# Kernel tuning notes

Hardware: AMD Instinct MI355X
Metric: run time of the kernel (lower is better)

The kernel has to match this reference:

```python
import jax, jax.numpy as jnp
import numpy as np

B, N, K, D = 2, 4096, 20, 128
PH = 8          # pos_mlp hidden dim
AH = 4 * D      # attn_mlp hidden dim (attn_mlp_hidden_mult=4)


def setup_inputs() -> dict:
    key = jax.random.key(0)
    ks = jax.random.split(key, 12)
    s = 0.02
    f32 = jnp.float32
    return {
        "x": jax.random.normal(ks[0], (B, N, 3), f32),
        "pos": jax.random.normal(ks[1], (B, N, 3), f32),
        # linear1/2/3 (torch Linear: y = x @ W.T + b)
        "W1": jax.random.normal(ks[2], (D, 3), f32) * s,  "b1": jnp.zeros((D,), f32),
        "W2": jax.random.normal(ks[3], (D, D), f32) * s,  "b2": jnp.zeros((D,), f32),
        "W3": jax.random.normal(ks[4], (D, D), f32) * s,  "b3": jnp.zeros((D,), f32),
        # PointTransformerLayer params
        "Wqkv": jax.random.normal(ks[5], (3 * D, D), f32) * s,          # to_qkv, no bias
        "Wp1": jax.random.normal(ks[6], (PH, 3), f32) * s,  "bp1": jnp.zeros((PH,), f32),
        "Wp2": jax.random.normal(ks[7], (D, PH), f32) * s,  "bp2": jnp.zeros((D,), f32),
        "Wa1": jax.random.normal(ks[8], (AH, D), f32) * s,  "ba1": jnp.zeros((AH,), f32),
        "Wa2": jax.random.normal(ks[9], (D, AH), f32) * s,  "ba2": jnp.zeros((D,), f32),
    }


def reference(x, pos, W1, b1, W2, b2, W3, b3, Wqkv,
              Wp1, bp1, Wp2, bp2, Wa1, ba1, Wa2, ba2):
    h = x @ W1.T + b1            # [B,N,D] linear1
    h1 = h @ W2.T + b2           # [B,N,D] linear2

    # --- PointTransformerLayer (lucidrains, KNN vector attention) ---
    qkv = h1 @ Wqkv.T            # [B,N,3D]
    q, k, v = jnp.split(qkv, 3, axis=-1)

    # squared pairwise distances and K nearest neighbors (self included)
    d2 = jnp.sum((pos[:, :, None, :] - pos[:, None, :, :]) ** 2, axis=-1)  # [B,N,N]
    _, idx = jax.lax.top_k(-d2, K)                                          # [B,N,K]

    gather = jax.vmap(lambda arr, ind: arr[ind])  # per-batch gather -> [B,N,K,*]
    kn = gather(k, idx)          # [B,N,K,D]
    vn = gather(v, idx)          # [B,N,K,D]
    pn = gather(pos, idx)        # [B,N,K,3]

    rel = pos[:, :, None, :] - pn                                   # [B,N,K,3]
    pe = jax.nn.relu(rel @ Wp1.T + bp1) @ Wp2.T + bp2               # pos_mlp [B,N,K,D]

    vn = vn + pe
    sim = jax.nn.relu((q[:, :, None, :] - kn + pe) @ Wa1.T + ba1) @ Wa2.T + ba2  # attn_mlp
    attn = jax.nn.softmax(sim, axis=2)                              # softmax over neighbors
    agg = jnp.sum(attn * vn, axis=2)                                # [B,N,D]

    return h + (agg @ W3.T + b3)  # residual: x + linear3(x1)
```

## Files before the change

kernel.cpp:

```cpp
#include <hip/hip_runtime.h>
#include <stdint.h>

#define BB 2
#define NN 4096
#define KNB 20
#define DD 128
#define PHH 8
#define AHH 512
#define BN (BB*NN)

typedef unsigned short ushort_t;
typedef short bf16x8 __attribute__((ext_vector_type(8)));
typedef float f32x4 __attribute__((ext_vector_type(4)));

__device__ __forceinline__ uint32_t umin32(uint32_t a, uint32_t b) { return a < b ? a : b; }
__device__ __forceinline__ uint32_t umax32(uint32_t a, uint32_t b) { return a > b ? a : b; }

__device__ __forceinline__ ushort_t f2bf(float f) {
    uint32_t x = __float_as_uint(f);
    return (ushort_t)((x + 0x7FFFu + ((x >> 16) & 1u)) >> 16);
}
__device__ __forceinline__ float bf2f(ushort_t u) {
    union { float f; uint32_t i; } c; c.i = ((uint32_t)u) << 16; return c.f;
}
__device__ __forceinline__ uint32_t cvt_pk_bf16(float lo, float hi) {
    uint32_t r;
    asm("v_cvt_pk_bf16_f32 %0, %1, %2" : "=v"(r) : "v"(lo), "v"(hi));
    return r;
}
__device__ __forceinline__ bf16x8 load_bfrag(const float* __restrict__ src) {
    float4 x = *(const float4*)src;
    float4 y = *(const float4*)(src + 4);
    union { bf16x8 v; uint32_t u[4]; } r;
    r.u[0] = cvt_pk_bf16(x.x, x.y);
    r.u[1] = cvt_pk_bf16(x.z, x.w);
    r.u[2] = cvt_pk_bf16(y.x, y.y);
    r.u[3] = cvt_pk_bf16(y.z, y.w);
    return r.v;
}

#define SW256(m, byteInRow) ((m)*256 + ((byteInRow) ^ (((m)&7) << 4)))
#define SW128(m, byteInRow) ((m)*128 + ((byteInRow) ^ (((m)&7) << 4)))

__global__ __launch_bounds__(256) void k_mega(
        const float* __restrict__ x, const float* __restrict__ pos,
        const float* __restrict__ W1, const float* __restrict__ b1,
        const float* __restrict__ W2f, const float* __restrict__ b2,
        const float* __restrict__ Wqkvf,
        const float* __restrict__ Wa1, const float* __restrict__ Wa2,
        float* __restrict__ h, ushort_t* __restrict__ qf,
        ushort_t* __restrict__ kf, ushort_t* __restrict__ vf,
        int* __restrict__ idx, ushort_t* __restrict__ wbf) {
    __shared__ __align__(16) char smem[16896];
    int tid = threadIdx.x, w = tid >> 6, lane = tid & 63;
    int bid = blockIdx.x;

    if (bid < BN/4) {
        int p = bid*4 + w;
        int b = p >> 12;
        float qx = pos[p*3+0], qy = pos[p*3+1], qz = pos[p*3+2];
        const float* pb = pos + (size_t)b*NN*3;
        uint32_t bk[KNB];
        #pragma unroll
        for (int i = 0; i < KNB; ++i) bk[i] = 0xFFFFFFFFu;
        for (int i = 0; i < NN/64; ++i) {
            int j = i*64 + lane;
            float dx = qx - pb[j*3+0];
            float dy = qy - pb[j*3+1];
            float dz = qz - pb[j*3+2];
            float d2 = dx*dx + dy*dy + dz*dz;
            uint32_t key = (__float_as_uint(d2) & 0xFFFFF000u) | (uint32_t)j;
            if (key < bk[KNB-1]) {
                uint32_t c = key;
                #pragma unroll
                for (int t = 0; t < KNB; ++t) {
                    uint32_t lo = umin32(c, bk[t]);
                    uint32_t hi = umax32(c, bk[t]);
                    bk[t] = lo; c = hi;
                }
            }
        }
        for (int r = 0; r < KNB; ++r) {
            uint32_t m = bk[0];
            #pragma unroll
            for (int s = 1; s < 64; s <<= 1)
                m = umin32(m, (uint32_t)__shfl_xor((int)m, s, 64));
            if (lane == 0) idx[(size_t)p*KNB + r] = (int)(m & 0xFFFu);
            bool win = (bk[0] == m);
            #pragma unroll
            for (int t = 0; t < KNB-1; ++t) bk[t] = win ? bk[t+1] : bk[t];
            bk[KNB-1] = win ? 0xFFFFFFFFu : bk[KNB-1];
        }
    } else if (bid < BN/4 + BN/32) {
        float* xs = (float*)(smem + 16384);
        int p0 = (bid - BN/4) * 32;
        if (tid < 96) xs[tid] = x[(size_t)p0*3 + tid];
        __syncthreads();

        #pragma unroll
        for (int it = 0; it < 16; ++it) {
            int lin = it*256 + tid;
            int m = lin >> 7, d = lin & 127;
            float hv = b1[d] + xs[m*3+0]*W1[d*3+0] + xs[m*3+1]*W1[d*3+1] + xs[m*3+2]*W1[d*3+2];
            h[(size_t)(p0+m)*DD + d] = hv;
            *(ushort_t*)&smem[SW256(m, d*2)] = f2bf(hv);
        }
        __syncthreads();

        {
            f32x4 acc[2][2];
            #pragma unroll
            for (int mt = 0; mt < 2; ++mt)
                #pragma unroll
                for (int ntl = 0; ntl < 2; ++ntl) acc[mt][ntl] = (f32x4){0,0,0,0};
            #pragma unroll
            for (int ks = 0; ks < 4; ++ks) {
                int k0 = ks*32 + (lane >> 4)*8;
                bf16x8 aF[2];
                #pragma unroll
                for (int mt = 0; mt < 2; ++mt)
                    aF[mt] = *(const bf16x8*)&smem[SW256(mt*16 + (lane & 15), k0*2)];
                #pragma unroll
                for (int ntl = 0; ntl < 2; ++ntl) {
                    int n = (2*w + ntl)*16 + (lane & 15);
                    bf16x8 bF = load_bfrag(W2f + (size_t)n*DD + k0);
                    #pragma unroll
                    for (int mt = 0; mt < 2; ++mt)
                        acc[mt][ntl] = __builtin_amdgcn_mfma_f32_16x16x32_bf16(aF[mt], bF, acc[mt][ntl], 0, 0, 0);
                }
            }
            #pragma unroll
            for (int ntl = 0; ntl < 2; ++ntl) {
                int n = (2*w + ntl)*16 + (lane & 15);
                float bias = b2[n];
                #pragma unroll
                for (int mt = 0; mt < 2; ++mt)
                    #pragma unroll
                    for (int i = 0; i < 4; ++i) {
                        int m = mt*16 + (lane >> 4)*4 + i;
                        *(ushort_t*)&smem[8192 + SW256(m, n*2)] = f2bf(acc[mt][ntl][i] + bias);
                    }
            }
        }
        __syncthreads();

        {
            f32x4 acc[2][6];
            #pragma unroll
            for (int mt = 0; mt < 2; ++mt)
                #pragma unroll
                for (int ntl = 0; ntl < 6; ++ntl) acc[mt][ntl] = (f32x4){0,0,0,0};
            #pragma unroll
            for (int ks = 0; ks < 4; ++ks) {
                int k0 = ks*32 + (lane >> 4)*8;
                bf16x8 aF[2];
                #pragma unroll
                for (int mt = 0; mt < 2; ++mt)
                    aF[mt] = *(const bf16x8*)&smem[8192 + SW256(mt*16 + (lane & 15), k0*2)];
                #pragma unroll
                for (int ntl = 0; ntl < 6; ++ntl) {
                    int n = (w*6 + ntl)*16 + (lane & 15);
                    bf16x8 bF = load_bfrag(Wqkvf + (size_t)n*DD + k0);
                    #pragma unroll
                    for (int mt = 0; mt < 2; ++mt)
                        acc[mt][ntl] = __builtin_amdgcn_mfma_f32_16x16x32_bf16(aF[mt], bF, acc[mt][ntl], 0, 0, 0);
                }
            }
            #pragma unroll
            for (int ntl = 0; ntl < 6; ++ntl) {
                int n = (w*6 + ntl)*16 + (lane & 15);
                int r = n >> 7, d = n & 127;
                ushort_t* dst = (r == 0) ? qf : (r == 1) ? kf : vf;
                #pragma unroll
                for (int mt = 0; mt < 2; ++mt)
                    #pragma unroll
                    for (int i = 0; i < 4; ++i) {
                        int m = mt*16 + (lane >> 4)*4 + i;
                        dst[(size_t)(p0+m)*DD + d] = f2bf(acc[mt][ntl][i]);
                    }
            }
        }
    } else {
        int base = (bid - (BN/4 + BN/32)) * 2048 + tid * 8;
        const float* src = (base < 65536) ? (Wa1 + base) : (Wa2 + (base - 65536));
        union { ushort_t u[8]; uint4 q; } pk;
        #pragma unroll
        for (int i = 0; i < 8; ++i) pk.u[i] = f2bf(src[i]);
        *(uint4*)&wbf[base] = pk.q;
    }
}

#define XL_OFF 0
#define TL_OFF 20480
#define PH_OFF 30720
#define NIDX_OFF 32000

__global__ __launch_bounds__(256, 4) void k_attn(
        const float* __restrict__ pos,
        const ushort_t* __restrict__ qf, const ushort_t* __restrict__ kf,
        const ushort_t* __restrict__ vf, const int* __restrict__ idx,
        const float* __restrict__ Wp1, const float* __restrict__ bp1,
        const float* __restrict__ Wp2, const float* __restrict__ bp2,
        const ushort_t* __restrict__ Wa1bf, const float* __restrict__ ba1,
        const ushort_t* __restrict__ Wa2bf, const float* __restrict__ ba2,
        float* __restrict__ agg) {
    __shared__ __align__(16) char smem[32320];
    int* nidx = (int*)(smem + NIDX_OFF);

    int tid = threadIdx.x, w = tid >> 6, lane = tid & 63;
    int lg = lane >> 4, c16 = lane & 15;
    int p0 = blockIdx.x * 4, b = p0 >> 12;

    if (tid < 80) nidx[tid] = idx[(size_t)(p0 + tid/20)*KNB + (tid%20)];
    __syncthreads();

    if (tid < 80) {
        int m = tid, g = m / 20;
        int j = nidx[m];
        const float* pq = pos + (size_t)(p0+g)*3;
        const float* pn = pos + (size_t)(b*NN+j)*3;
        float r0 = pq[0]-pn[0], r1 = pq[1]-pn[1], r2 = pq[2]-pn[2];
        union { ushort_t u[8]; uint4 q; } pk;
        #pragma unroll
        for (int jj = 0; jj < PHH; ++jj) {
            float a = bp1[jj] + r0*Wp1[jj*3+0] + r1*Wp1[jj*3+1] + r2*Wp1[jj*3+2];
            pk.u[jj] = f2bf(fmaxf(a, 0.f));
        }
        *(uint4*)&smem[PH_OFF + m*16] = pk.q;
    }
    __syncthreads();

    int dA = w*32 + c16, dB = w*32 + 16 + c16;
    float bp2A = bp2[dA], bp2B = bp2[dB];
    float ba2A = ba2[dA], ba2B = ba2[dB];

    bf16x8 bP0 = {0,0,0,0,0,0,0,0}, bP1 = {0,0,0,0,0,0,0,0};
    if (lg == 0) {
        bP0 = load_bfrag(Wp2 + (size_t)dA*PHH);
        bP1 = load_bfrag(Wp2 + (size_t)dB*PHH);
    }

    float qv[4][2];
    #pragma unroll
    for (int g = 0; g < 4; ++g) {
        qv[g][0] = bf2f(qf[(size_t)(p0+g)*DD + dA]);
        qv[g][1] = bf2f(qf[(size_t)(p0+g)*DD + dB]);
    }

    uint32_t vpe_pk[5][4];

    #pragma unroll
    for (int mt = 0; mt < 5; ++mt) {
        bf16x8 aP = {0,0,0,0,0,0,0,0};
        if (lg == 0) aP = *(const bf16x8*)&smem[PH_OFF + (mt*16 + c16)*16];
        f32x4 accP0 = (f32x4){0,0,0,0}, accP1 = (f32x4){0,0,0,0};
        accP0 = __builtin_amdgcn_mfma_f32_16x16x32_bf16(aP, bP0, accP0, 0, 0, 0);
        accP1 = __builtin_amdgcn_mfma_f32_16x16x32_bf16(aP, bP1, accP1, 0, 0, 0);
        float qsA = (mt==0) ? qv[0][0]
                  : (mt==1) ? (lg>=1 ? qv[1][0] : qv[0][0])
                  : (mt==2) ? (lg>=2 ? qv[2][0] : qv[1][0])
                  : (mt==3) ? (lg==3 ? qv[3][0] : qv[2][0])
                  : qv[3][0];
        float qsB = (mt==0) ? qv[0][1]
                  : (mt==1) ? (lg>=1 ? qv[1][1] : qv[0][1])
                  : (mt==2) ? (lg>=2 ? qv[2][1] : qv[1][1])
                  : (mt==3) ? (lg==3 ? qv[3][1] : qv[2][1])
                  : qv[3][1];
        #pragma unroll
        for (int i = 0; i < 4; ++i) {
            int m = mt*16 + lg*4 + i;
            int j = nidx[m];
            const ushort_t* kr = kf + (size_t)(b*NN+j)*DD;
            const ushort_t* vr = vf + (size_t)(b*NN+j)*DD;
            float peA = accP0[i] + bp2A;
            float peB = accP1[i] + bp2B;
            *(ushort_t*)&smem[XL_OFF + SW256(m, dA*2)] = f2bf(qsA - bf2f(kr[dA]) + peA);
            *(ushort_t*)&smem[XL_OFF + SW256(m, dB*2)] = f2bf(qsB - bf2f(kr[dB]) + peB);
            vpe_pk[mt][i] = cvt_pk_bf16(bf2f(vr[dA]) + peA, bf2f(vr[dB]) + peB);
        }
    }
    __syncthreads();

    f32x4 accS[5][2];
    #pragma unroll
    for (int mt = 0; mt < 5; ++mt)
        #pragma unroll
        for (int ntl = 0; ntl < 2; ++ntl) accS[mt][ntl] = (f32x4){0,0,0,0};

    for (int c = 0; c < 8; ++c) {
        f32x4 accB[5];
        #pragma unroll
        for (int mt = 0; mt < 5; ++mt) accB[mt] = (f32x4){0,0,0,0};
        #pragma unroll
        for (int ks = 0; ks < 4; ++ks) {
            int k0 = ks*32 + lg*8;
            bf16x8 aF[5];
            #pragma unroll
            for (int mt = 0; mt < 5; ++mt)
                aF[mt] = *(const bf16x8*)&smem[XL_OFF + SW256(mt*16 + c16, k0*2)];
            bf16x8 bF = *(const bf16x8*)&Wa1bf[(size_t)(c*64 + w*16 + c16)*DD + k0];
            #pragma unroll
            for (int mt = 0; mt < 5; ++mt)
                accB[mt] = __builtin_amdgcn_mfma_f32_16x16x32_bf16(aF[mt], bF, accB[mt], 0, 0, 0);
        }
        {
            int al = w*16 + c16;
            float bias = ba1[c*64 + al];
            #pragma unroll
            for (int mt = 0; mt < 5; ++mt)
                #pragma unroll
                for (int i = 0; i < 4; ++i) {
                    int m = mt*16 + lg*4 + i;
                    *(ushort_t*)&smem[TL_OFF + SW128(m, al*2)] = f2bf(fmaxf(accB[mt][i] + bias, 0.f));
                }
        }
        __syncthreads();

        #pragma unroll
        for (int ks = 0; ks < 2; ++ks) {
            int k0 = ks*32 + lg*8;
            bf16x8 aF[5];
            #pragma unroll
            for (int mt = 0; mt < 5; ++mt)
                aF[mt] = *(const bf16x8*)&smem[TL_OFF + SW128(mt*16 + c16, k0*2)];
            #pragma unroll
            for (int ntl = 0; ntl < 2; ++ntl) {
                int dd = w*32 + ntl*16 + c16;
                bf16x8 bF = *(const bf16x8*)&Wa2bf[(size_t)dd*AHH + c*64 + k0];
                #pragma unroll
                for (int mt = 0; mt < 5; ++mt)
                    accS[mt][ntl] = __builtin_amdgcn_mfma_f32_16x16x32_bf16(aF[mt], bF, accS[mt][ntl], 0, 0, 0);
            }
        }
        __syncthreads();
    }

    float s_mtA[5], a_mtA[5], s_mtB[5], a_mtB[5];
    #pragma unroll
    for (int mt = 0; mt < 5; ++mt) {
        float sa = 0.f, aa = 0.f, sb = 0.f, ab = 0.f;
        #pragma unroll
        for (int i = 0; i < 4; ++i) {
            float eA = __expf(accS[mt][0][i] + ba2A);
            float eB = __expf(accS[mt][1][i] + ba2B);
            uint32_t pk = vpe_pk[mt][i];
            float vA = bf2f((ushort_t)(pk & 0xFFFFu));
            float vB = bf2f((ushort_t)(pk >> 16));
            sa += eA; aa += eA*vA;
            sb += eB; ab += eB*vB;
        }
        s_mtA[mt] = sa; a_mtA[mt] = aa; s_mtB[mt] = sb; a_mtB[mt] = ab;
    }
    bool eq0 = (lg==0), ge1 = (lg>=1), ge2 = (lg>=2), le1 = (lg<=1), le2 = (lg<=2), eq3 = (lg==3);
    float s0A = s_mtA[0] + (eq0 ? s_mtA[1] : 0.f);
    float s1A = (ge1 ? s_mtA[1] : 0.f) + (le1 ? s_mtA[2] : 0.f);
    float s2A = (ge2 ? s_mtA[2] : 0.f) + (le2 ? s_mtA[3] : 0.f);
    float s3A = (eq3 ? s_mtA[3] : 0.f) + s_mtA[4];
    float a0A = a_mtA[0] + (eq0 ? a_mtA[1] : 0.f);
    float a1A = (ge1 ? a_mtA[1] : 0.f) + (le1 ? a_mtA[2] : 0.f);
    float a2A = (ge2 ? a_mtA[2] : 0.f) + (le2 ? a_mtA[3] : 0.f);
    float a3A = (eq3 ? a_mtA[3] : 0.f) + a_mtA[4];
    float s0B = s_mtB[0] + (eq0 ? s_mtB[1] : 0.f);
    float s1B = (ge1 ? s_mtB[1] : 0.f) + (le1 ? s_mtB[2] : 0.f);
    float s2B = (ge2 ? s_mtB[2] : 0.f) + (le2 ? s_mtB[3] : 0.f);
    float s3B = (eq3 ? s_mtB[3] : 0.f) + s_mtB[4];
    float a0B = a_mtB[0] + (eq0 ? a_mtB[1] : 0.f);
    float a1B = (ge1 ? a_mtB[1] : 0.f) + (le1 ? a_mtB[2] : 0.f);
    float a2B = (ge2 ? a_mtB[2] : 0.f) + (le2 ? a_mtB[3] : 0.f);
    float a3B = (eq3 ? a_mtB[3] : 0.f) + a_mtB[4];

    #define RED2(v) { v += __shfl_xor(v, 16, 64); v += __shfl_xor(v, 32, 64); }
    RED2(s0A) RED2(s1A) RED2(s2A) RED2(s3A)
    RED2(a0A) RED2(a1A) RED2(a2A) RED2(a3A)
    RED2(s0B) RED2(s1B) RED2(s2B) RED2(s3B)
    RED2(a0B) RED2(a1B) RED2(a2B) RED2(a3B)
    #undef RED2

    float myS_A = (lg==0) ? s0A : (lg==1) ? s1A : (lg==2) ? s2A : s3A;
    float myA_A = (lg==0) ? a0A : (lg==1) ? a1A : (lg==2) ? a2A : a3A;
    float myS_B = (lg==0) ? s0B : (lg==1) ? s1B : (lg==2) ? s2B : s3B;
    float myA_B = (lg==0) ? a0B : (lg==1) ? a1B : (lg==2) ? a2B : a3B;
    agg[(size_t)(p0+lg)*DD + dA] = myA_A / myS_A;
    agg[(size_t)(p0+lg)*DD + dB] = myA_B / myS_B;
}

__global__ __launch_bounds__(256) void k_out(
        const float* __restrict__ agg, const float* __restrict__ h,
        const float* __restrict__ W3f, const float* __restrict__ b3,
        float* __restrict__ out) {
    __shared__ __align__(16) char smem[8192];
    int tid = threadIdx.x, w = tid >> 6, lane = tid & 63;
    int p0 = blockIdx.x * 32;

    #pragma unroll
    for (int it = 0; it < 16; ++it) {
        int lin = it*256 + tid;
        int m = lin >> 7, d = lin & 127;
        *(ushort_t*)&smem[SW256(m, d*2)] = f2bf(agg[(size_t)(p0+m)*DD + d]);
    }
    __syncthreads();

    f32x4 acc[2][2];
    #pragma unroll
    for (int mt = 0; mt < 2; ++mt)
        #pragma unroll
        for (int ntl = 0; ntl < 2; ++ntl) acc[mt][ntl] = (f32x4){0,0,0,0};
    #pragma unroll
    for (int ks = 0; ks < 4; ++ks) {
        int k0 = ks*32 + (lane >> 4)*8;
        bf16x8 aF[2];
        #pragma unroll
        for (int mt = 0; mt < 2; ++mt)
            aF[mt] = *(const bf16x8*)&smem[SW256(mt*16 + (lane & 15), k0*2)];
        #pragma unroll
        for (int ntl = 0; ntl < 2; ++ntl) {
            int n = (2*w + ntl)*16 + (lane & 15);
            bf16x8 bF = load_bfrag(W3f + (size_t)n*DD + k0);
            #pragma unroll
            for (int mt = 0; mt < 2; ++mt)
                acc[mt][ntl] = __builtin_amdgcn_mfma_f32_16x16x32_bf16(aF[mt], bF, acc[mt][ntl], 0, 0, 0);
        }
    }
    #pragma unroll
    for (int ntl = 0; ntl < 2; ++ntl) {
        int n = (2*w + ntl)*16 + (lane & 15);
        float bias = b3[n];
        #pragma unroll
        for (int mt = 0; mt < 2; ++mt)
            #pragma unroll
            for (int i = 0; i < 4; ++i) {
                int m = mt*16 + (lane >> 4)*4 + i;
                size_t o = (size_t)(p0+m)*DD + n;
                out[o] = acc[mt][ntl][i] + bias + h[o];
            }
    }
}

extern "C" void kernel_launch(void* const* d_in, const int* in_sizes, int n_in,
                              void* d_out, int out_size, void* d_ws, size_t ws_size,
                              hipStream_t stream) {
    const float* x    = (const float*)d_in[0];
    const float* pos  = (const float*)d_in[1];
    const float* W1   = (const float*)d_in[2];
    const float* b1   = (const float*)d_in[3];
    const float* W2   = (const float*)d_in[4];
    const float* b2   = (const float*)d_in[5];
    const float* W3   = (const float*)d_in[6];
    const float* b3   = (const float*)d_in[7];
    const float* Wqkv = (const float*)d_in[8];
    const float* Wp1  = (const float*)d_in[9];
    const float* bp1  = (const float*)d_in[10];
    const float* Wp2  = (const float*)d_in[11];
    const float* bp2  = (const float*)d_in[12];
    const float* Wa1  = (const float*)d_in[13];
    const float* ba1  = (const float*)d_in[14];
    const float* Wa2  = (const float*)d_in[15];
    const float* ba2  = (const float*)d_in[16];

    float* ws = (float*)d_ws;
    float* h   = ws;
    float* agg = ws + (size_t)BN*DD;
    ushort_t* qf = (ushort_t*)(ws + 2*(size_t)BN*DD);
    ushort_t* kf = qf + (size_t)BN*DD;
    ushort_t* vf = qf + 2*(size_t)BN*DD;
    int* idx = (int*)((char*)d_ws + 14680064);
    ushort_t* wbf = (ushort_t*)((char*)d_ws + 15335424);
    ushort_t* Wa1bf = wbf;
    ushort_t* Wa2bf = wbf + 65536;

    k_mega<<<BN/4 + BN/32 + 64, 256, 0, stream>>>(x, pos, W1, b1, W2, b2, Wqkv,
                                                  Wa1, Wa2, h, qf, kf, vf, idx, wbf);
    k_attn<<<BN/4, 256, 0, stream>>>(pos, qf, kf, vf, idx,
                                     Wp1, bp1, Wp2, bp2, Wa1bf, ba1, Wa2bf, ba2, agg);
    k_out <<<BN/32, 256, 0, stream>>>(agg, h, W3, b3, (float*)d_out);
}
```

Before: 175.1 us.

## Fuse output projection into attention kernel and widen attn-MLP hidden chunk

Removes the separate k_out kernel. Its linear3 projection plus residual now runs at the end of k_attn as a padded 16-row MFMA over the 4 points of each block, using W3 pre-converted to bf16 in k_mega. The attention MLP now processes hidden chunks of 128 instead of 64, which halves the number of barrier rounds at the cost of more LDS (occupancy hint drops from 4 to 3) and more accumulators. s_setprio hints are added around the MFMA sections. The fused output GEMM wastes 12 of 16 MFMA rows but avoids the agg round trip through global memory and one launch.

```diff
diff --git a/kernel.cpp b/kernel.cpp
--- a/kernel.cpp
+++ b/kernel.cpp
@@ -40,7 +40,6 @@
 }
 
 #define SW256(m, byteInRow) ((m)*256 + ((byteInRow) ^ (((m)&7) << 4)))
-#define SW128(m, byteInRow) ((m)*128 + ((byteInRow) ^ (((m)&7) << 4)))
 
 __global__ __launch_bounds__(256) void k_mega(
         const float* __restrict__ x, const float* __restrict__ pos,
@@ -48,6 +47,7 @@
         const float* __restrict__ W2f, const float* __restrict__ b2,
         const float* __restrict__ Wqkvf,
         const float* __restrict__ Wa1, const float* __restrict__ Wa2,
+        const float* __restrict__ W3,
         float* __restrict__ h, ushort_t* __restrict__ qf,
         ushort_t* __restrict__ kf, ushort_t* __restrict__ vf,
         int* __restrict__ idx, ushort_t* __restrict__ wbf) {
@@ -182,7 +182,9 @@
         }
     } else {
         int base = (bid - (BN/4 + BN/32)) * 2048 + tid * 8;
-        const float* src = (base < 65536) ? (Wa1 + base) : (Wa2 + (base - 65536));
+        const float* src = (base < 65536) ? (Wa1 + base)
+                        : (base < 131072) ? (Wa2 + (base - 65536))
+                        : (W3 + (base - 131072));
         union { ushort_t u[8]; uint4 q; } pk;
         #pragma unroll
         for (int i = 0; i < 8; ++i) pk.u[i] = f2bf(src[i]);
@@ -192,10 +194,10 @@
 
 #define XL_OFF 0
 #define TL_OFF 20480
-#define PH_OFF 30720
-#define NIDX_OFF 32000
-
-__global__ __launch_bounds__(256, 4) void k_attn(
+#define PH_OFF 40960
+#define NIDX_OFF 42240
+
+__global__ __launch_bounds__(256, 3) void k_attn(
         const float* __restrict__ pos,
         const ushort_t* __restrict__ qf, const ushort_t* __restrict__ kf,
         const ushort_t* __restrict__ vf, const int* __restrict__ idx,
@@ -203,8 +205,9 @@
         const float* __restrict__ Wp2, const float* __restrict__ bp2,
         const ushort_t* __restrict__ Wa1bf, const float* __restrict__ ba1,
         const ushort_t* __restrict__ Wa2bf, const float* __restrict__ ba2,
-        float* __restrict__ agg) {
-    __shared__ __align__(16) char smem[32320];
+        const ushort_t* __restrict__ W3bf, const float* __restrict__ b3,
+        const float* __restrict__ h, float* __restrict__ out) {
+    __shared__ __align__(16) char smem[42560];
     int* nidx = (int*)(smem + NIDX_OFF);
 
     int tid = threadIdx.x, w = tid >> 6, lane = tid & 63;
@@ -287,10 +290,13 @@
         #pragma unroll
         for (int ntl = 0; ntl < 2; ++ntl) accS[mt][ntl] = (f32x4){0,0,0,0};
 
-    for (int c = 0; c < 8; ++c) {
-        f32x4 accB[5];
-        #pragma unroll
-        for (int mt = 0; mt < 5; ++mt) accB[mt] = (f32x4){0,0,0,0};
+    for (int c = 0; c < 4; ++c) {
+        f32x4 accB[5][2];
+        #pragma unroll
+        for (int mt = 0; mt < 5; ++mt)
+            #pragma unroll
+            for (int ntl = 0; ntl < 2; ++ntl) accB[mt][ntl] = (f32x4){0,0,0,0};
+        __builtin_amdgcn_s_setprio(1);
         #pragma unroll
         for (int ks = 0; ks < 4; ++ks) {
             int k0 = ks*32 + lg*8;
@@ -298,40 +304,47 @@
             #pragma unroll
             for (int mt = 0; mt < 5; ++mt)
                 aF[mt] = *(const bf16x8*)&smem[XL_OFF + SW256(mt*16 + c16, k0*2)];
-            bf16x8 bF = *(const bf16x8*)&Wa1bf[(size_t)(c*64 + w*16 + c16)*DD + k0];
-            #pragma unroll
-            for (int mt = 0; mt < 5; ++mt)
-                accB[mt] = __builtin_amdgcn_mfma_f32_16x16x32_bf16(aF[mt], bF, accB[mt], 0, 0, 0);
-        }
-        {
-            int al = w*16 + c16;
-            float bias = ba1[c*64 + al];
+            #pragma unroll
+            for (int ntl = 0; ntl < 2; ++ntl) {
+                bf16x8 bF = *(const bf16x8*)&Wa1bf[(size_t)(c*128 + w*32 + ntl*16 + c16)*DD + k0];
+                #pragma unroll
+                for (int mt = 0; mt < 5; ++mt)
+                    accB[mt][ntl] = __builtin_amdgcn_mfma_f32_16x16x32_bf16(aF[mt], bF, accB[mt][ntl], 0, 0, 0);
+            }
+        }
+        __builtin_amdgcn_s_setprio(0);
+        #pragma unroll
+        for (int ntl = 0; ntl < 2; ++ntl) {
+            int al = w*32 + ntl*16 + c16;
+            float bias = ba1[c*128 + al];
             #pragma unroll
             for (int mt = 0; mt < 5; ++mt)
                 #pragma unroll
                 for (int i = 0; i < 4; ++i) {
                     int m = mt*16 + lg*4 + i;
-                    *(ushort_t*)&smem[TL_OFF + SW128(m, al*2)] = f2bf(fmaxf(accB[mt][i] + bias, 0.f));
+                    *(ushort_t*)&smem[TL_OFF + SW256(m, al*2)] = f2bf(fmaxf(accB[mt][ntl][i] + bias, 0.f));
                 }
         }
         __syncthreads();
 
-        #pragma unroll
-        for (int ks = 0; ks < 2; ++ks) {
+        __builtin_amdgcn_s_setprio(1);
+        #pragma unroll
+        for (int ks = 0; ks < 4; ++ks) {
             int k0 = ks*32 + lg*8;
             bf16x8 aF[5];
             #pragma unroll
             for (int mt = 0; mt < 5; ++mt)
-                aF[mt] = *(const bf16x8*)&smem[TL_OFF + SW128(mt*16 + c16, k0*2)];
+                aF[mt] = *(const bf16x8*)&smem[TL_OFF + SW256(mt*16 + c16, k0*2)];
             #pragma unroll
             for (int ntl = 0; ntl < 2; ++ntl) {
                 int dd = w*32 + ntl*16 + c16;
-                bf16x8 bF = *(const bf16x8*)&Wa2bf[(size_t)dd*AHH + c*64 + k0];
+                bf16x8 bF = *(const bf16x8*)&Wa2bf[(size_t)dd*AHH + c*128 + k0];
                 #pragma unroll
                 for (int mt = 0; mt < 5; ++mt)
                     accS[mt][ntl] = __builtin_amdgcn_mfma_f32_16x16x32_bf16(aF[mt], bF, accS[mt][ntl], 0, 0, 0);
             }
         }
+        __builtin_amdgcn_s_setprio(0);
         __syncthreads();
     }
 
@@ -380,59 +393,40 @@
     float myA_A = (lg==0) ? a0A : (lg==1) ? a1A : (lg==2) ? a2A : a3A;
     float myS_B = (lg==0) ? s0B : (lg==1) ? s1B : (lg==2) ? s2B : s3B;
     float myA_B = (lg==0) ? a0B : (lg==1) ? a1B : (lg==2) ? a2B : a3B;
-    agg[(size_t)(p0+lg)*DD + dA] = myA_A / myS_A;
-    agg[(size_t)(p0+lg)*DD + dB] = myA_B / myS_B;
-}
-
-__global__ __launch_bounds__(256) void k_out(
-        const float* __restrict__ agg, const float* __restrict__ h,
-        const float* __restrict__ W3f, const float* __restrict__ b3,
-        float* __restrict__ out) {
-    __shared__ __align__(16) char smem[8192];
-    int tid = threadIdx.x, w = tid >> 6, lane = tid & 63;
-    int p0 = blockIdx.x * 32;
-
-    #pragma unroll
-    for (int it = 0; it < 16; ++it) {
-        int lin = it*256 + tid;
-        int m = lin >> 7, d = lin & 127;
-        *(ushort_t*)&smem[SW256(m, d*2)] = f2bf(agg[(size_t)(p0+m)*DD + d]);
-    }
+    float aggA = myA_A / myS_A;
+    float aggB = myA_B / myS_B;
+
+    #pragma unroll
+    for (int z = 0; z < 3; ++z)
+        *(uint32_t*)&smem[XL_OFF + 1024 + (z*256 + tid)*4] = 0u;
+    *(ushort_t*)&smem[XL_OFF + SW256(lg, dA*2)] = f2bf(aggA);
+    *(ushort_t*)&smem[XL_OFF + SW256(lg, dB*2)] = f2bf(aggB);
     __syncthreads();
 
-    f32x4 acc[2][2];
-    #pragma unroll
-    for (int mt = 0; mt < 2; ++mt)
-        #pragma unroll
-        for (int ntl = 0; ntl < 2; ++ntl) acc[mt][ntl] = (f32x4){0,0,0,0};
+    f32x4 accO[2];
+    accO[0] = (f32x4){0,0,0,0}; accO[1] = (f32x4){0,0,0,0};
     #pragma unroll
     for (int ks = 0; ks < 4; ++ks) {
-        int k0 = ks*32 + (lane >> 4)*8;
-        bf16x8 aF[2];
-        #pragma unroll
-        for (int mt = 0; mt < 2; ++mt)
-            aF[mt] = *(const bf16x8*)&smem[SW256(mt*16 + (lane & 15), k0*2)];
+        int k0 = ks*32 + lg*8;
+        bf16x8 aF = *(const bf16x8*)&smem[XL_OFF + SW256(c16, k0*2)];
         #pragma unroll
         for (int ntl = 0; ntl < 2; ++ntl) {
-            int n = (2*w + ntl)*16 + (lane & 15);
-            bf16x8 bF = load_bfrag(W3f + (size_t)n*DD + k0);
-            #pragma unroll
-            for (int mt = 0; mt < 2; ++mt)
-                acc[mt][ntl] = __builtin_amdgcn_mfma_f32_16x16x32_bf16(aF[mt], bF, acc[mt][ntl], 0, 0, 0);
-        }
-    }
-    #pragma unroll
-    for (int ntl = 0; ntl < 2; ++ntl) {
-        int n = (2*w + ntl)*16 + (lane & 15);
-        float bias = b3[n];
-        #pragma unroll
-        for (int mt = 0; mt < 2; ++mt)
+            int n = (w*2 + ntl)*16 + c16;
+            bf16x8 bF = *(const bf16x8*)&W3bf[(size_t)n*DD + k0];
+            accO[ntl] = __builtin_amdgcn_mfma_f32_16x16x32_bf16(aF, bF, accO[ntl], 0, 0, 0);
+        }
+    }
+    if (lg == 0) {
+        #pragma unroll
+        for (int ntl = 0; ntl < 2; ++ntl) {
+            int n = (w*2 + ntl)*16 + c16;
+            float bias = b3[n];
             #pragma unroll
             for (int i = 0; i < 4; ++i) {
-                int m = mt*16 + (lane >> 4)*4 + i;
-                size_t o = (size_t)(p0+m)*DD + n;
-                out[o] = acc[mt][ntl][i] + bias + h[o];
-            }
+                size_t o = (size_t)(p0+i)*DD + n;
+                out[o] = accO[ntl][i] + bias + h[o];
+            }
+        }
     }
 }
 
@@ -459,7 +453,6 @@
 
     float* ws = (float*)d_ws;
     float* h   = ws;
-    float* agg = ws + (size_t)BN*DD;
     ushort_t* qf = (ushort_t*)(ws + 2*(size_t)BN*DD);
     ushort_t* kf = qf + (size_t)BN*DD;
     ushort_t* vf = qf + 2*(size_t)BN*DD;
@@ -467,10 +460,11 @@
     ushort_t* wbf = (ushort_t*)((char*)d_ws + 15335424);
     ushort_t* Wa1bf = wbf;
     ushort_t* Wa2bf = wbf + 65536;
-
-    k_mega<<<BN/4 + BN/32 + 64, 256, 0, stream>>>(x, pos, W1, b1, W2, b2, Wqkv,
-                                                  Wa1, Wa2, h, qf, kf, vf, idx, wbf);
+    ushort_t* W3bf  = wbf + 131072;
+
+    k_mega<<<BN/4 + BN/32 + 72, 256, 0, stream>>>(x, pos, W1, b1, W2, b2, Wqkv,
+                                                  Wa1, Wa2, W3, h, qf, kf, vf, idx, wbf);
     k_attn<<<BN/4, 256, 0, stream>>>(pos, qf, kf, vf, idx,
-                                     Wp1, bp1, Wp2, bp2, Wa1bf, ba1, Wa2bf, ba2, agg);
-    k_out <<<BN/32, 256, 0, stream>>>(agg, h, W3, b3, (float*)d_out);
-}
+                                     Wp1, bp1, Wp2, bp2, Wa1bf, ba1, Wa2bf, ba2,
+                                     W3bf, b3, h, (float*)d_out);
+}
```

New measurement: 221.5 us. 1.26x slower.
